# Kernel optimization log

Measured on AMD Instinct MI355X. Metric: run time of the kernel, lower is better.

The kernel has to match this reference:

```python
import jax, jax.numpy as jnp
import numpy as np

B, T, E = 4, 2048, 2048
NH, NKV, HD = 16, 4, 128
THETA = 10000.0


def _rope(x, pos_ids, theta):
    # x: [b, h, t, hd]; pos_ids: [b, t]; theta: [hd/2]
    ang = pos_ids[:, None, :, None].astype(jnp.float32) * theta  # [b,1,t,hd/2]
    cos, sin = jnp.cos(ang), jnp.sin(ang)
    x1, x2 = x[..., ::2], x[..., 1::2]
    # interleave rotated pairs back to [..., hd]
    rot = jnp.stack([x1 * cos - x2 * sin, x1 * sin + x2 * cos], axis=-1)
    return rot.reshape(x.shape)


def setup_inputs() -> dict:
    key = jax.random.key(0)
    ks = jax.random.split(key, 10)
    s = 0.02
    x = jax.random.normal(ks[0], (B, T, E), dtype=jnp.float32)
    attention_mask = jax.random.randint(ks[1], (B, T, T), 0, 2, dtype=jnp.int32)
    # torch nn.Linear weights stored here as [in, out] (y = x @ W + b)
    Wq = jax.random.normal(ks[2], (E, E), dtype=jnp.float32) * s
    bq = jnp.zeros((E,), dtype=jnp.float32)
    Wk = jax.random.normal(ks[3], (E, NKV * HD), dtype=jnp.float32) * s
    bk = jnp.zeros((NKV * HD,), dtype=jnp.float32)
    Wv = jax.random.normal(ks[4], (E, NKV * HD), dtype=jnp.float32) * s
    bv = jnp.zeros((NKV * HD,), dtype=jnp.float32)
    Wo = jax.random.normal(ks[5], (E, E), dtype=jnp.float32) * s
    bo = jnp.zeros((E,), dtype=jnp.float32)
    return {"x": x, "attention_mask": attention_mask, "Wq": Wq, "bq": bq,
            "Wk": Wk, "bk": bk, "Wv": Wv, "bv": bv, "Wo": Wo, "bo": bo}


def reference(x, attention_mask, Wq, bq, Wk, bk, Wv, bv, Wo, bo):
    b, t = x.shape[0], x.shape[1]
    # faithful to original: plain reshape (view), NOT transpose-based head split
    q = (x @ Wq + bq).reshape(b, NH, t, HD)
    k = (x @ Wk + bk).reshape(b, NKV, t, HD)
    v = (x @ Wv + bv).reshape(b, NKV, t, HD)
    theta = THETA ** (-jnp.arange(0, HD, 2, dtype=jnp.float32) / HD)
    pos = jnp.broadcast_to(jnp.arange(t), (b, t))
    # original RoPE.forward is wrapped in @torch.no_grad() -> stop_gradient
    k = jax.lax.stop_gradient(_rope(k, pos, theta))
    v = jax.lax.stop_gradient(_rope(v, pos, theta))  # note: RoPE applied to V too
    g = NH // NKV
    k = jnp.tile(k, (1, g, 1, 1))  # torch .repeat tiles kv heads
    v = jnp.tile(v, (1, g, 1, 1))
    # original divides by head_dim ** (-0.5) == multiply by sqrt(head_dim)
    scores = jnp.einsum('bhqd,bhkd->bhqk', q, k) * (HD ** 0.5)
    scores = jnp.where(attention_mask[:, None, :, :] == 0, jnp.float32(1e-9), scores)
    attn = jax.nn.softmax(scores, axis=-1)  # dropout inactive (eval mode)
    out = jnp.einsum('bhqk,bhkd->bhqd', attn, v)
    out = out.transpose(0, 2, 1, 3).reshape(b, t, NH * HD)
    return out @ Wo + bo
```

## Files before the change

kernel.cpp:

```cpp
#include <hip/hip_runtime.h>
#include <math.h>

constexpr int Bc   = 4;
constexpr int Tc   = 2048;
constexpr int Ec   = 2048;
constexpr int NHc  = 16;
constexpr int NKVc = 4;
constexpr int HDc  = 128;
constexpr int KVEc = NKVc * HDc;

typedef __attribute__((ext_vector_type(8))) short bf16x8;
typedef __attribute__((ext_vector_type(4))) short short4v;
typedef __attribute__((ext_vector_type(4))) float f32x4;

__device__ __forceinline__ short f2bf(float f) {
    union { float f; unsigned u; } v; v.f = f;
    unsigned r = v.u + 0x7FFF + ((v.u >> 16) & 1);
    return (short)(r >> 16);
}
__device__ __forceinline__ float bf2f(short s) {
    union { unsigned u; float f; } v; v.u = ((unsigned)(unsigned short)s) << 16;
    return v.f;
}
__device__ __forceinline__ float ex2(float x) {
    float r; asm("v_exp_f32 %0, %1" : "=v"(r) : "v"(x)); return r;
}
__device__ __forceinline__ void gload16(const void* g, void* l) {
    __builtin_amdgcn_global_load_lds(
        (const __attribute__((address_space(1))) unsigned*)g,
        (__attribute__((address_space(3))) unsigned*)l, 16, 0, 0);
}

__global__ __launch_bounds__(256)
void convert_split(const float* __restrict__ X, short* __restrict__ Xhi,
                   short* __restrict__ Xlo)
{
    int i = blockIdx.x * 256 + threadIdx.x;
    float4 v = ((const float4*)X)[i];
    float fv[4] = {v.x, v.y, v.z, v.w};
    short4v hi, lo;
    #pragma unroll
    for (int j = 0; j < 4; ++j) {
        hi[j] = f2bf(fv[j]);
        lo[j] = f2bf(fv[j] - bf2f(hi[j]));
    }
    ((short4v*)Xhi)[i] = hi;
    ((short4v*)Xlo)[i] = lo;
}

__global__ __launch_bounds__(256)
void transpose_split(const float* __restrict__ W, short* __restrict__ WThi,
                     short* __restrict__ WTlo, int K, int N)
{
    __shared__ float Ls[32][33];
    const int k0 = blockIdx.x * 32, n0 = blockIdx.y * 32;
    const int t = threadIdx.x;
    const int r = t >> 3, c4 = (t & 7) << 2;
    float4 v = *(const float4*)(W + (size_t)(k0 + r) * N + n0 + c4);
    Ls[r][c4 + 0] = v.x; Ls[r][c4 + 1] = v.y;
    Ls[r][c4 + 2] = v.z; Ls[r][c4 + 3] = v.w;
    __syncthreads();
    short4v hi, lo;
    #pragma unroll
    for (int i = 0; i < 4; ++i) {
        float f = Ls[c4 + i][r];
        hi[i] = f2bf(f);
        lo[i] = f2bf(f - bf2f(hi[i]));
    }
    *(short4v*)(WThi + (size_t)(n0 + r) * K + k0 + c4) = hi;
    if (WTlo) *(short4v*)(WTlo + (size_t)(n0 + r) * K + k0 + c4) = lo;
}

__global__ __launch_bounds__(256)
void mask_bits(const int* __restrict__ mask, unsigned long long* __restrict__ Mb)
{
    const int widx = blockIdx.x * 4 + (threadIdx.x >> 6);
    const int L = threadIdx.x & 63;
    const int m = mask[(size_t)widx * 64 + L];
    unsigned long long bits = __ballot(m != 0);
    if (L == 0) Mb[widx] = bits;
}

template <bool SPLIT>
__global__ __launch_bounds__(256, 2)
void gemm_mfma(const short* __restrict__ Ahi, const short* __restrict__ Alo,
               const short* __restrict__ Bhi, const short* __restrict__ Blo,
               const float* __restrict__ bias, float* __restrict__ C,
               int M, int N, int K)
{
    __shared__ short AsH[128 * 32];
    __shared__ short BsH[128 * 32];
    __shared__ short AsL[SPLIT ? 128 * 32 : 8];
    __shared__ short BsL[SPLIT ? 128 * 32 : 8];

    const int t = threadIdx.x;
    const int w = t >> 6, L = t & 63;
    const int l16 = L & 15, quad = L >> 4;
    const int wr = w >> 1, wc = w & 1;
    const int bm = blockIdx.x * 128, bn = blockIdx.y * 128;

    const int sm = L >> 2;
    const int sq = ((L & 3) - (sm >> 2)) & 3;
    const int scol = sq * 8;

    f32x4 acc[4][4];
    #pragma unroll
    for (int mi = 0; mi < 4; ++mi)
        #pragma unroll
        for (int ni = 0; ni < 4; ++ni) acc[mi][ni] = (f32x4){0, 0, 0, 0};

    const int fxor = (quad + (l16 >> 2)) & 3;

    for (int k0 = 0; k0 < K; k0 += 32) {
        __syncthreads();
        #pragma unroll
        for (int i = 0; i < 2; ++i) {
            const int wl = w * 2 + i;
            const size_t ra = (size_t)(bm + wl * 16 + sm) * K + k0 + scol;
            const size_t rb = (size_t)(bn + wl * 16 + sm) * K + k0 + scol;
            gload16(Ahi + ra, &AsH[wl * 512]);
            gload16(Bhi + rb, &BsH[wl * 512]);
            if (SPLIT) {
                gload16(Alo + ra, &AsL[wl * 512]);
                gload16(Blo + rb, &BsL[wl * 512]);
            }
        }
        __syncthreads();

        bf16x8 ah[4], bh[4], al[4], bl[4];
        #pragma unroll
        for (int mi = 0; mi < 4; ++mi) {
            const int ch = ((wr * 4 + mi) * 64 + l16 * 4 + fxor) * 8;
            ah[mi] = *(const bf16x8*)&AsH[ch];
            if (SPLIT) al[mi] = *(const bf16x8*)&AsL[ch];
        }
        #pragma unroll
        for (int ni = 0; ni < 4; ++ni) {
            const int ch = ((wc * 4 + ni) * 64 + l16 * 4 + fxor) * 8;
            bh[ni] = *(const bf16x8*)&BsH[ch];
            if (SPLIT) bl[ni] = *(const bf16x8*)&BsL[ch];
        }
        #pragma unroll
        for (int mi = 0; mi < 4; ++mi)
            #pragma unroll
            for (int ni = 0; ni < 4; ++ni) {
                acc[mi][ni] = __builtin_amdgcn_mfma_f32_16x16x32_bf16(
                    ah[mi], bh[ni], acc[mi][ni], 0, 0, 0);
                if (SPLIT) {
                    acc[mi][ni] = __builtin_amdgcn_mfma_f32_16x16x32_bf16(
                        al[mi], bh[ni], acc[mi][ni], 0, 0, 0);
                    acc[mi][ni] = __builtin_amdgcn_mfma_f32_16x16x32_bf16(
                        ah[mi], bl[ni], acc[mi][ni], 0, 0, 0);
                }
            }
    }

    #pragma unroll
    for (int ni = 0; ni < 4; ++ni) {
        const int col = bn + wc * 64 + ni * 16 + l16;
        const float bv = bias[col];
        #pragma unroll
        for (int mi = 0; mi < 4; ++mi) {
            #pragma unroll
            for (int r = 0; r < 4; ++r) {
                const int row = bm + wr * 64 + mi * 16 + quad * 4 + r;
                C[(size_t)row * N + col] = acc[mi][ni][r] + bv;
            }
        }
    }
}

__global__ __launch_bounds__(256)
void rope_k(const float* __restrict__ X2d, short* __restrict__ Khi,
            short* __restrict__ Klo)
{
    const int idx = blockIdx.x * 256 + threadIdx.x;
    const int j  = idx & 63;
    const int tk = (idx >> 6) & (Tc - 1);
    const int kh = (idx >> 17) & (NKVc - 1);
    const int bb = idx >> 19;
    const int row = (kh << 9) + (tk >> 2);
    const int col = ((tk & 3) << 7) + (j << 1);
    const float* src = X2d + ((size_t)bb * Tc + row) * KVEc + col;
    const float a = src[0];
    const float b = src[1];
    const float theta = powf(10000.0f, -(float)j * (1.0f / 64.0f));
    const float ang = (float)tk * theta;
    float s, c;
    sincosf(ang, &s, &c);
    const float r0 = a * c - b * s;
    const float r1 = a * s + b * c;
    const size_t off = (((size_t)bb * NKVc + kh) * Tc + tk) * HDc + (j << 1);
    short h0 = f2bf(r0), h1 = f2bf(r1);
    Khi[off]     = h0;  Klo[off]     = f2bf(r0 - bf2f(h0));
    Khi[off + 1] = h1;  Klo[off + 1] = f2bf(r1 - bf2f(h1));
}

__global__ __launch_bounds__(256)
void rope_v_t(const float* __restrict__ V2d, short* __restrict__ Vt)
{
    __shared__ short Ls[128][40];
    const int g  = blockIdx.x;
    const int kh = blockIdx.y;
    const int bb = blockIdx.z;
    const int t  = threadIdx.x;

    const float* src = V2d + ((size_t)bb * Tc + (kh << 9) + (g << 3)) * KVEc;
    #pragma unroll
    for (int i = 0; i < 4; ++i) {
        int e = i * 256 + t;
        float4 v = ((const float4*)src)[e];
        int row = e >> 7;
        int col = (e & 127) << 2;
        int tkl = (row << 2) + (col >> 7);
        int d0  = col & 127;
        int tk  = (g << 5) + tkl;
        float fv[4] = {v.x, v.y, v.z, v.w};
        #pragma unroll
        for (int p = 0; p < 2; ++p) {
            int j = (d0 >> 1) + p;
            float theta = powf(10000.0f, -(float)j * (1.0f / 64.0f));
            float ang = (float)tk * theta;
            float s, c;
            sincosf(ang, &s, &c);
            float a = fv[2 * p], b = fv[2 * p + 1];
            Ls[d0 + 2 * p    ][tkl] = f2bf(a * c - b * s);
            Ls[d0 + 2 * p + 1][tkl] = f2bf(a * s + b * c);
        }
    }
    __syncthreads();
    const int d = t >> 1;
    const int h16 = (t & 1) << 4;
    short* dst = Vt + (((size_t)bb * NKVc + kh) * HDc + d) * Tc + (g << 5) + h16;
    bf16x8 o0 = *(const bf16x8*)&Ls[d][h16];
    bf16x8 o1 = *(const bf16x8*)&Ls[d][h16 + 8];
    *(bf16x8*)dst = o0;
    *(bf16x8*)(dst + 8) = o1;
}

__global__ __launch_bounds__(256, 3)
void attn_mfma(const float* __restrict__ Q2d, const short* __restrict__ Khi_g,
               const short* __restrict__ Klo_g, const short* __restrict__ Vt_g,
               const unsigned long long* __restrict__ Mb, short* __restrict__ AObf)
{
    __shared__ short KhiS[64 * 128];
    __shared__ short KloS[64 * 128];
    __shared__ short VtS [128 * 64];

    const int fid  = blockIdx.x + 32 * (blockIdx.y + 16 * blockIdx.z);
    const int slot = fid >> 3;
    const int grp  = (fid & 7) + 8 * (slot >> 5);
    const int qb   = slot & 31;
    const int h    = grp & 15;
    const int bb   = grp >> 4;

    const int t    = threadIdx.x;
    const int w    = t >> 6;
    const int L    = t & 63;
    const int l16  = L & 15;
    const int quad = L >> 4;
    const int q1v  = quad >> 1;
    const int kh   = h & (NKVc - 1);
    const int tq0  = qb * 64 + w * 16;

    bf16x8 qhi[4], qlo[4];
    {
        const float* qrow = Q2d +
            ((size_t)(bb * Tc + h * HDc + qb * 4 + w)) * Ec + 128 * l16;
        #pragma unroll
        for (int kc = 0; kc < 4; ++kc) {
            const float* p = qrow + kc * 32 + quad * 8;
            #pragma unroll
            for (int j = 0; j < 8; ++j) {
                float f = p[j];
                short hi = f2bf(f);
                qhi[kc][j] = hi;
                qlo[kc][j] = f2bf(f - bf2f(hi));
            }
        }
    }

    float m_r = -INFINITY, lp = 0.0f;
    f32x4 o[8];
    #pragma unroll
    for (int nc = 0; nc < 8; ++nc) o[nc] = (f32x4){0, 0, 0, 0};

    const short* kbh = Khi_g + ((size_t)(bb * NKVc + kh)) * Tc * HDc;
    const short* kbl = Klo_g + ((size_t)(bb * NKVc + kh)) * Tc * HDc;
    const short* vb  = Vt_g  + ((size_t)(bb * NKVc + kh)) * HDc * Tc;
    const unsigned long long* mrow =
        Mb + ((size_t)(bb * Tc + tq0 + l16)) * (Tc / 64);

    constexpr float SCALE2  = 11.313708498984761f * 1.4426950408889634f;
    constexpr float MASKED2 = 1e-9f * 1.4426950408889634f;

    const int km   = L >> 4;
    const int kpos = L & 15;
    const int vm   = L >> 3;
    const int vc   = ((L & 7) - vm) & 7;

    const int srcA = l16 + 16 * ((2 * quad)     & 3);
    const int srcB = l16 + 16 * ((2 * quad + 1) & 3);

    for (int kt = 0; kt < Tc / 64; ++kt) {
        const unsigned long long mw = mrow[kt];

        __syncthreads();

        #pragma unroll
        for (int i = 0; i < 4; ++i) {
            const int wl = w * 4 + i;
            const int krow = wl * 4 + km;
            const int kc_ = (kpos - (krow & 15)) & 15;
            const size_t go = (size_t)(kt * 64 + krow) * HDc + kc_ * 8;
            gload16(kbh + go, &KhiS[wl * 512]);
            gload16(kbl + go, &KloS[wl * 512]);
            const int vrow = wl * 8 + vm;
            gload16(vb + (size_t)vrow * Tc + kt * 64 + vc * 8, &VtS[wl * 512]);
        }
        __syncthreads();

        f32x4 s[4];
        __builtin_amdgcn_s_setprio(1);
        #pragma unroll
        for (int nt = 0; nt < 4; ++nt) {
            f32x4 acc = (f32x4){0, 0, 0, 0};
            #pragma unroll
            for (int kc = 0; kc < 4; ++kc) {
                const int ch = (((nt * 4 + (l16 >> 2)) << 6) + ((l16 & 3) << 4)
                                + ((kc * 4 + quad + l16) & 15)) << 3;
                bf16x8 khiF = *(const bf16x8*)&KhiS[ch];
                bf16x8 kloF = *(const bf16x8*)&KloS[ch];
                acc = __builtin_amdgcn_mfma_f32_16x16x32_bf16(khiF, qhi[kc], acc, 0, 0, 0);
                acc = __builtin_amdgcn_mfma_f32_16x16x32_bf16(khiF, qlo[kc], acc, 0, 0, 0);
                acc = __builtin_amdgcn_mfma_f32_16x16x32_bf16(kloF, qhi[kc], acc, 0, 0, 0);
            }
            s[nt] = acc;
        }
        __builtin_amdgcn_s_setprio(0);

        const unsigned mlo = (unsigned)mw;
        const unsigned mhi = (unsigned)(mw >> 32);
        const int gq = quad << 2;
        const unsigned fm[4] = { mlo >> gq, (mlo >> 16) >> gq,
                                 mhi >> gq, (mhi >> 16) >> gq };
        #pragma unroll
        for (int nt = 0; nt < 4; ++nt)
            #pragma unroll
            for (int r = 0; r < 4; ++r)
                s[nt][r] = (fm[nt] & (1u << r)) ? s[nt][r] * SCALE2 : MASKED2;

        float mt;
        {
            float a0 = fmaxf(fmaxf(s[0][0], s[0][1]), fmaxf(s[0][2], s[0][3]));
            float a1 = fmaxf(fmaxf(s[1][0], s[1][1]), fmaxf(s[1][2], s[1][3]));
            float a2 = fmaxf(fmaxf(s[2][0], s[2][1]), fmaxf(s[2][2], s[2][3]));
            float a3 = fmaxf(fmaxf(s[3][0], s[3][1]), fmaxf(s[3][2], s[3][3]));
            mt = fmaxf(fmaxf(a0, a1), fmaxf(a2, a3));
        }
        mt = fmaxf(mt, __shfl_xor(mt, 16));
        mt = fmaxf(mt, __shfl_xor(mt, 32));
        const float mn  = fmaxf(m_r, mt);
        const float alq = ex2(m_r - mn);
        m_r = mn;

        float rs;
        {
            float t0 = 0.f, t1 = 0.f;
            #pragma unroll
            for (int nt = 0; nt < 4; ++nt) {
                float p0 = ex2(s[nt][0] - mn);
                float p1 = ex2(s[nt][1] - mn);
                float p2 = ex2(s[nt][2] - mn);
                float p3 = ex2(s[nt][3] - mn);
                s[nt][0] = p0; s[nt][1] = p1; s[nt][2] = p2; s[nt][3] = p3;
                t0 += p0 + p1; t1 += p2 + p3;
            }
            rs = t0 + t1;
        }

        if (__any(alq < 1.0f)) {
            lp *= alq;
            float alo[4];
            #pragma unroll
            for (int r = 0; r < 4; ++r)
                alo[r] = __shfl(alq, quad * 16 + quad * 4 + r);
            #pragma unroll
            for (int nc = 0; nc < 8; ++nc)
                #pragma unroll
                for (int r = 0; r < 4; ++r)
                    o[nc][r] *= alo[r];
        }
        lp += rs;

        int pk00, pk01, pk10, pk11, pk20, pk21, pk30, pk31;
        asm("v_cvt_pk_bf16_f32 %0, %1, %2" : "=v"(pk00) : "v"(s[0][0]), "v"(s[0][1]));
        asm("v_cvt_pk_bf16_f32 %0, %1, %2" : "=v"(pk01) : "v"(s[0][2]), "v"(s[0][3]));
        asm("v_cvt_pk_bf16_f32 %0, %1, %2" : "=v"(pk10) : "v"(s[1][0]), "v"(s[1][1]));
        asm("v_cvt_pk_bf16_f32 %0, %1, %2" : "=v"(pk11) : "v"(s[1][2]), "v"(s[1][3]));
        asm("v_cvt_pk_bf16_f32 %0, %1, %2" : "=v"(pk20) : "v"(s[2][0]), "v"(s[2][1]));
        asm("v_cvt_pk_bf16_f32 %0, %1, %2" : "=v"(pk21) : "v"(s[2][2]), "v"(s[2][3]));
        asm("v_cvt_pk_bf16_f32 %0, %1, %2" : "=v"(pk30) : "v"(s[3][0]), "v"(s[3][1]));
        asm("v_cvt_pk_bf16_f32 %0, %1, %2" : "=v"(pk31) : "v"(s[3][2]), "v"(s[3][3]));

        union U { int d[4]; bf16x8 v; } A0, A1;
        {
            int u0, u1;
            u0 = __shfl(pk00, srcA); u1 = __shfl(pk10, srcA); A0.d[0] = q1v ? u1 : u0;
            u0 = __shfl(pk01, srcA); u1 = __shfl(pk11, srcA); A0.d[1] = q1v ? u1 : u0;
            u0 = __shfl(pk00, srcB); u1 = __shfl(pk10, srcB); A0.d[2] = q1v ? u1 : u0;
            u0 = __shfl(pk01, srcB); u1 = __shfl(pk11, srcB); A0.d[3] = q1v ? u1 : u0;
            u0 = __shfl(pk20, srcA); u1 = __shfl(pk30, srcA); A1.d[0] = q1v ? u1 : u0;
            u0 = __shfl(pk21, srcA); u1 = __shfl(pk31, srcA); A1.d[1] = q1v ? u1 : u0;
            u0 = __shfl(pk20, srcB); u1 = __shfl(pk30, srcB); A1.d[2] = q1v ? u1 : u0;
            u0 = __shfl(pk21, srcB); u1 = __shfl(pk31, srcB); A1.d[3] = q1v ? u1 : u0;
        }

        __builtin_amdgcn_s_setprio(1);
        #pragma unroll
        for (int nc = 0; nc < 8; ++nc) {
            const int rg = (nc * 2 + (l16 >> 3)) << 6;
            const int rm = l16 & 7;
            const int ch0 = (rg + (rm << 3) + ((quad + rm) & 7)) << 3;
            const int ch1 = (rg + (rm << 3) + ((quad + 4 + rm) & 7)) << 3;
            bf16x8 b0 = *(const bf16x8*)&VtS[ch0];
            bf16x8 b1 = *(const bf16x8*)&VtS[ch1];
            o[nc] = __builtin_amdgcn_mfma_f32_16x16x32_bf16(A0.v, b0, o[nc], 0, 0, 0);
            o[nc] = __builtin_amdgcn_mfma_f32_16x16x32_bf16(A1.v, b1, o[nc], 0, 0, 0);
        }
        __builtin_amdgcn_s_setprio(0);
    }

    lp += __shfl_xor(lp, 16);
    lp += __shfl_xor(lp, 32);
    const float invl = 1.0f / lp;
    float invo[4];
    #pragma unroll
    for (int r = 0; r < 4; ++r)
        invo[r] = __shfl(invl, quad * 16 + quad * 4 + r);

    #pragma unroll
    for (int r = 0; r < 4; ++r) {
        short* orow = AObf + ((size_t)(bb * Tc + tq0 + quad * 4 + r)) * Ec
                           + h * HDc + l16;
        #pragma unroll
        for (int nc = 0; nc < 8; ++nc)
            orow[nc * 16] = f2bf(o[nc][r] * invo[r]);
    }
}

extern "C" void kernel_launch(void* const* d_in, const int* in_sizes, int n_in,
                              void* d_out, int out_size, void* d_ws, size_t ws_size,
                              hipStream_t stream)
{
    const float* x    = (const float*)d_in[0];
    const int*  amask = (const int*)  d_in[1];
    const float* Wq   = (const float*)d_in[2];
    const float* bq   = (const float*)d_in[3];
    const float* Wk   = (const float*)d_in[4];
    const float* bk   = (const float*)d_in[5];
    const float* Wv   = (const float*)d_in[6];
    const float* bv   = (const float*)d_in[7];
    const float* Wo   = (const float*)d_in[8];
    const float* bo   = (const float*)d_in[9];
    float* out = (float*)d_out;

    char* ws = (char*)d_ws;
    float* Q2d   = (float*)(ws);
    short* Xhi   = (short*)(ws + 67108864);
    short* Xlo   = (short*)(ws + 100663296);
    short* WqThi = (short*)(ws + 134217728);
    short* WqTlo = (short*)(ws + 134217728 + 8388608);
    float* K2d   = (float*)(ws + 150994944);
    float* V2d   = (float*)(ws + 100663296);
    short* Khi   = (short*)(ws + 100663296 + 16777216);
    short* Klo   = (short*)(ws + 100663296 + 25165824);
    short* WkThi = (short*)(ws + 134217728);
    short* WkTlo = (short*)(ws + 134217728 + 2097152);
    short* WvThi = (short*)(ws + 134217728 + 4194304);
    short* WoThi = (short*)(ws + 134217728 + 8388608);
    short* Vt    = (short*)(ws + 150994944);
    short* AObf  = (short*)(ws + 67108864);
    unsigned long long* Mb = (unsigned long long*)(ws + 167772160);

    const int M = Bc * Tc;
    dim3 blk(256);

    mask_bits<<<(Bc * Tc * (Tc / 64)) / 4, blk, 0, stream>>>(amask, Mb);
    transpose_split<<<dim3(Ec / 32, Ec / 32), blk, 0, stream>>>(Wq, WqThi, WqTlo, Ec, Ec);
    convert_split<<<(M * Ec / 4) / 256, blk, 0, stream>>>(x, Xhi, Xlo);
    gemm_mfma<true><<<dim3(M / 128, Ec / 128), blk, 0, stream>>>(
        Xhi, Xlo, WqThi, WqTlo, bq, Q2d, M, Ec, Ec);
    transpose_split<<<dim3(Ec / 32, KVEc / 32), blk, 0, stream>>>(Wk, WkThi, WkTlo, Ec, KVEc);
    transpose_split<<<dim3(Ec / 32, KVEc / 32), blk, 0, stream>>>(Wv, WvThi, nullptr, Ec, KVEc);
    transpose_split<<<dim3(Ec / 32, Ec / 32), blk, 0, stream>>>(Wo, WoThi, nullptr, Ec, Ec);
    gemm_mfma<true><<<dim3(M / 128, KVEc / 128), blk, 0, stream>>>(
        Xhi, Xlo, WkThi, WkTlo, bk, K2d, M, KVEc, Ec);
    gemm_mfma<false><<<dim3(M / 128, KVEc / 128), blk, 0, stream>>>(
        Xhi, nullptr, WvThi, nullptr, bv, V2d, M, KVEc, Ec);
    rope_k<<<(Bc * NKVc * Tc * 64) / 256, blk, 0, stream>>>(K2d, Khi, Klo);
    rope_v_t<<<dim3(Tc / 32, NKVc, Bc), blk, 0, stream>>>(V2d, Vt);
    attn_mfma<<<dim3(Tc / 64, NHc, Bc), blk, 0, stream>>>(
        Q2d, Khi, Klo, Vt, Mb, AObf);
    gemm_mfma<false><<<dim3(M / 128, Ec / 128), blk, 0, stream>>>(
        AObf, nullptr, WoThi, nullptr, bo, out, M, Ec, Ec);
}
```

Baseline: 1.127 ms.

## Split K/V staging to overlap next-tile loads with softmax and PV compute

Breaks the per-tile K and V global-to-LDS loads into separate stages. The next K tile is issued after QK^T and the next V tile after PV, with explicit vmcnt waits and barriers so that loads overlap compute instead of sitting behind a full sync. It also adds a lazy-rescale softmax that only updates the running max when it grows by more than 8 (log2 units), which skips most o-accumulator rescales. The cost is fragile hand-tuned waitcnt counts, one redundant wraparound prefetch on the last iteration, and exponentials that can reach up to 2^8 before normalisation.

After: 1.059 ms. 6.0% less time.

```diff
diff --git a/kernel.cpp b/kernel.cpp
--- a/kernel.cpp
+++ b/kernel.cpp
@@ -302,11 +302,7 @@
     const int srcA = l16 + 16 * ((2 * quad)     & 3);
     const int srcB = l16 + 16 * ((2 * quad + 1) & 3);
 
-    for (int kt = 0; kt < Tc / 64; ++kt) {
-        const unsigned long long mw = mrow[kt];
-
-        __syncthreads();
-
+    auto stageK = [&](int kt) {
         #pragma unroll
         for (int i = 0; i < 4; ++i) {
             const int wl = w * 4 + i;
@@ -315,13 +311,31 @@
             const size_t go = (size_t)(kt * 64 + krow) * HDc + kc_ * 8;
             gload16(kbh + go, &KhiS[wl * 512]);
             gload16(kbl + go, &KloS[wl * 512]);
+        }
+    };
+    auto stageV = [&](int kt) {
+        #pragma unroll
+        for (int i = 0; i < 4; ++i) {
+            const int wl = w * 4 + i;
             const int vrow = wl * 8 + vm;
             gload16(vb + (size_t)vrow * Tc + kt * 64 + vc * 8, &VtS[wl * 512]);
         }
-        __syncthreads();
+    };
+
+    asm volatile("s_waitcnt vmcnt(0)" ::: "memory");
+    stageK(0);
+    __builtin_amdgcn_sched_barrier(0);
+    stageV(0);
+    unsigned long long mw = mrow[0];
+
+    for (int kt = 0; kt < Tc / 64; ++kt) {
+        const int ktn = (kt + 1) & 31;
+
+        asm volatile("s_waitcnt vmcnt(5)" ::: "memory");
+        __builtin_amdgcn_s_barrier();
+        __builtin_amdgcn_sched_barrier(0);
 
         f32x4 s[4];
-        __builtin_amdgcn_s_setprio(1);
         #pragma unroll
         for (int nt = 0; nt < 4; ++nt) {
             f32x4 acc = (f32x4){0, 0, 0, 0};
@@ -337,7 +351,13 @@
             }
             s[nt] = acc;
         }
-        __builtin_amdgcn_s_setprio(0);
+
+        asm volatile("s_waitcnt lgkmcnt(0)" ::: "memory");
+        __builtin_amdgcn_sched_barrier(0);
+        __builtin_amdgcn_s_barrier();
+        __builtin_amdgcn_sched_barrier(0);
+        stageK(ktn);
+        __builtin_amdgcn_sched_barrier(0);
 
         const unsigned mlo = (unsigned)mw;
         const unsigned mhi = (unsigned)(mw >> 32);
@@ -360,36 +380,37 @@
         }
         mt = fmaxf(mt, __shfl_xor(mt, 16));
         mt = fmaxf(mt, __shfl_xor(mt, 32));
-        const float mn  = fmaxf(m_r, mt);
-        const float alq = ex2(m_r - mn);
-        m_r = mn;
+
+        const bool res = (mt > m_r + 8.0f);
+        if (__any(res)) {
+            const float mn_ = res ? mt : m_r;
+            const float alq = ex2(m_r - mn_);
+            m_r = mn_;
+            lp *= alq;
+            float alo[4];
+            #pragma unroll
+            for (int r = 0; r < 4; ++r)
+                alo[r] = __shfl(alq, quad * 16 + quad * 4 + r);
+            #pragma unroll
+            for (int nc = 0; nc < 8; ++nc)
+                #pragma unroll
+                for (int r = 0; r < 4; ++r)
+                    o[nc][r] *= alo[r];
+        }
 
         float rs;
         {
             float t0 = 0.f, t1 = 0.f;
             #pragma unroll
             for (int nt = 0; nt < 4; ++nt) {
-                float p0 = ex2(s[nt][0] - mn);
-                float p1 = ex2(s[nt][1] - mn);
-                float p2 = ex2(s[nt][2] - mn);
-                float p3 = ex2(s[nt][3] - mn);
+                float p0 = ex2(s[nt][0] - m_r);
+                float p1 = ex2(s[nt][1] - m_r);
+                float p2 = ex2(s[nt][2] - m_r);
+                float p3 = ex2(s[nt][3] - m_r);
                 s[nt][0] = p0; s[nt][1] = p1; s[nt][2] = p2; s[nt][3] = p3;
                 t0 += p0 + p1; t1 += p2 + p3;
             }
             rs = t0 + t1;
-        }
-
-        if (__any(alq < 1.0f)) {
-            lp *= alq;
-            float alo[4];
-            #pragma unroll
-            for (int r = 0; r < 4; ++r)
-                alo[r] = __shfl(alq, quad * 16 + quad * 4 + r);
-            #pragma unroll
-            for (int nc = 0; nc < 8; ++nc)
-                #pragma unroll
-                for (int r = 0; r < 4; ++r)
-                    o[nc][r] *= alo[r];
         }
         lp += rs;
 
@@ -416,7 +437,10 @@
             u0 = __shfl(pk21, srcB); u1 = __shfl(pk31, srcB); A1.d[3] = q1v ? u1 : u0;
         }
 
-        __builtin_amdgcn_s_setprio(1);
+        asm volatile("s_waitcnt vmcnt(8)" ::: "memory");
+        __builtin_amdgcn_s_barrier();
+        __builtin_amdgcn_sched_barrier(0);
+
         #pragma unroll
         for (int nc = 0; nc < 8; ++nc) {
             const int rg = (nc * 2 + (l16 >> 3)) << 6;
@@ -428,8 +452,16 @@
             o[nc] = __builtin_amdgcn_mfma_f32_16x16x32_bf16(A0.v, b0, o[nc], 0, 0, 0);
             o[nc] = __builtin_amdgcn_mfma_f32_16x16x32_bf16(A1.v, b1, o[nc], 0, 0, 0);
         }
-        __builtin_amdgcn_s_setprio(0);
-    }
+
+        asm volatile("s_waitcnt lgkmcnt(0)" ::: "memory");
+        __builtin_amdgcn_sched_barrier(0);
+        __builtin_amdgcn_s_barrier();
+        __builtin_amdgcn_sched_barrier(0);
+        stageV(ktn);
+        mw = mrow[ktn];
+    }
+
+    asm volatile("s_waitcnt vmcnt(0)" ::: "memory");
 
     lp += __shfl_xor(lp, 16);
     lp += __shfl_xor(lp, 32);
```
